# Kernel optimization log

Hardware: AMD Instinct MI355X
Metric: run time of the kernel (lower is better)

## Reference

```python
import jax, jax.numpy as jnp
import numpy as np

N_NODES = 50000
N_EDGES = 640000
N_REL = 8
D_IN = 128
D_HID = 128
D_OUT = 64


def setup_inputs() -> dict:
    key = jax.random.key(0)
    ks = jax.random.split(key, 10)
    x = jax.random.normal(ks[0], (N_NODES, D_IN), dtype=jnp.float32)
    edge_src = jax.random.randint(ks[1], (N_EDGES,), 0, N_NODES, dtype=jnp.int32)
    edge_dst = jax.random.randint(ks[2], (N_EDGES,), 0, N_NODES, dtype=jnp.int32)
    edge_type = jax.random.randint(ks[3], (N_EDGES,), 0, N_REL, dtype=jnp.int32)
    # Glorot-ish scaling for stability
    W1 = jax.random.normal(ks[4], (N_REL, D_IN, D_HID), dtype=jnp.float32) / np.sqrt(D_IN)
    root1 = jax.random.normal(ks[5], (D_IN, D_HID), dtype=jnp.float32) / np.sqrt(D_IN)
    b1 = jnp.zeros((D_HID,), dtype=jnp.float32)
    W2 = jax.random.normal(ks[6], (N_REL, D_HID, D_OUT), dtype=jnp.float32) / np.sqrt(D_HID)
    root2 = jax.random.normal(ks[7], (D_HID, D_OUT), dtype=jnp.float32) / np.sqrt(D_HID)
    b2 = jnp.zeros((D_OUT,), dtype=jnp.float32)
    return {"x": x, "edge_src": edge_src, "edge_dst": edge_dst, "edge_type": edge_type,
            "W1": W1, "root1": root1, "b1": b1, "W2": W2, "root2": root2, "b2": b2}


def rgcn_conv(x, edge_src, edge_dst, edge_type, W, W_root, b):
    """RGCNConv with default per-relation mean aggregation + root weight + bias."""
    N = x.shape[0]
    R, _, O = W.shape
    # Transform all nodes under all relation weights once: [N, R, O]
    xW = jnp.einsum('nd,rdo->nro', x, W)
    # Gather per-edge relation-specific messages: [E, O]
    msg = xW[edge_src, edge_type]
    # Segment per (dst, relation) for mean aggregation
    seg = edge_dst.astype(jnp.int32) * R + edge_type.astype(jnp.int32)
    cnt = jax.ops.segment_sum(jnp.ones_like(edge_type, dtype=x.dtype), seg, num_segments=N * R)
    agg = jax.ops.segment_sum(msg, seg, num_segments=N * R)  # [N*R, O]
    agg = agg / jnp.maximum(cnt, 1.0)[:, None]
    rel_sum = agg.reshape(N, R, O).sum(axis=1)  # [N, O]
    return rel_sum + x @ W_root + b


def reference(x, edge_src, edge_dst, edge_type, W1, root1, b1, W2, root2, b2):
    h = rgcn_conv(x, edge_src, edge_dst, edge_type, W1, root1, b1)
    h = rgcn_conv(h, edge_src, edge_dst, edge_type, W2, root2, b2)
    return jax.nn.sigmoid(h)
```

## Files before the change

### kernel.cpp

```cpp
#include <hip/hip_runtime.h>
#include <math.h>

#define NN 50000
#define NE 640000
#define NR 8
#define SCAN_N (NN * NR)
#define SCAN_CH 2048
#define SCAN_NB ((SCAN_N + SCAN_CH - 1) / SCAN_CH)

typedef __attribute__((ext_vector_type(8))) _Float16 half8;
typedef __attribute__((ext_vector_type(8))) short short8;
typedef __attribute__((ext_vector_type(4))) float f32x4;
typedef const void __attribute__((address_space(1))) gvoid_t;
typedef void __attribute__((address_space(3))) svoid_t;

__device__ __forceinline__ unsigned short f2h(float f) {
    _Float16 h = (_Float16)f;
    return __builtin_bit_cast(unsigned short, h);
}
__device__ __forceinline__ float h2f(unsigned short u) {
    return (float)__builtin_bit_cast(_Float16, u);
}

__global__ __launch_bounds__(256) void count_kernel(const int* __restrict__ dst,
                                                    const int* __restrict__ typ,
                                                    int* __restrict__ cnt, int E) {
    int e = blockIdx.x * 256 + threadIdx.x;
    if (e < E) atomicAdd(&cnt[dst[e] * NR + typ[e]], 1);
}

__global__ __launch_bounds__(256) void inv_kernel(const int* __restrict__ cnt,
                                                  float* __restrict__ inv, int n) {
    int i = blockIdx.x * 256 + threadIdx.x;
    if (i < n) {
        int c = cnt[i];
        inv[i] = 1.0f / (float)(c > 1 ? c : 1);
    }
}

__global__ __launch_bounds__(256) void scan1_kernel(const int* __restrict__ cnt,
                                                    int* __restrict__ loc,
                                                    int* __restrict__ bsum) {
    __shared__ int s[256];
    const int t = threadIdx.x;
    const int base = blockIdx.x * SCAN_CH + t * 8;
    int v[8];
    int sum = 0;
#pragma unroll
    for (int j = 0; j < 8; ++j) {
        int idx = base + j;
        v[j] = (idx < SCAN_N) ? cnt[idx] : 0;
        sum += v[j];
    }
    s[t] = sum;
    __syncthreads();
    for (int off = 1; off < 256; off <<= 1) {
        int u = (t >= off) ? s[t - off] : 0;
        __syncthreads();
        s[t] += u;
        __syncthreads();
    }
    int run = (t == 0) ? 0 : s[t - 1];
#pragma unroll
    for (int j = 0; j < 8; ++j) {
        int idx = base + j;
        if (idx < SCAN_N) loc[idx] = run;
        run += v[j];
    }
    if (t == 255) bsum[blockIdx.x] = s[255];
}

__global__ __launch_bounds__(256) void scan2_kernel(const int* __restrict__ bsum,
                                                    int* __restrict__ boff, int nb) {
    __shared__ int s[256];
    const int t = threadIdx.x;
    s[t] = (t < nb) ? bsum[t] : 0;
    __syncthreads();
    for (int off = 1; off < 256; off <<= 1) {
        int u = (t >= off) ? s[t - off] : 0;
        __syncthreads();
        s[t] += u;
        __syncthreads();
    }
    if (t < nb) boff[t] = (t == 0) ? 0 : s[t - 1];
    if (t == nb - 1) boff[nb] = s[t];
}

__global__ __launch_bounds__(256) void scan3_kernel(int* __restrict__ rowptr,
                                                    int* __restrict__ start,
                                                    const int* __restrict__ boff, int nb) {
    const int b = blockIdx.x, t = threadIdx.x;
    const int add = boff[b];
#pragma unroll
    for (int j = 0; j < 8; ++j) {
        int idx = b * SCAN_CH + t * 8 + j;
        if (idx < SCAN_N) {
            int v = rowptr[idx] + add;
            rowptr[idx] = v;
            start[idx] = v;
        }
    }
    if (b == 0 && t == 0) rowptr[SCAN_N] = boff[nb];
}

__global__ __launch_bounds__(256) void fill_kernel(const int* __restrict__ src,
                                                   const int* __restrict__ dst,
                                                   const int* __restrict__ typ,
                                                   int* __restrict__ start,
                                                   int* __restrict__ srcrel, int E) {
    int e = blockIdx.x * 256 + threadIdx.x;
    if (e >= E) return;
    int r = typ[e];
    int pos = atomicAdd(&start[dst[e] * NR + r], 1);
    srcrel[pos] = src[e] | (r << 20);
}

__global__ __launch_bounds__(256) void cvt_kernel(const float* __restrict__ x,
                                                  unsigned short* __restrict__ xh, int n4) {
    int i = blockIdx.x * 256 + threadIdx.x;
    if (i >= n4) return;
    float4 v = ((const float4*)x)[i];
    uint2 u;
    u.x = (unsigned)f2h(v.x) | ((unsigned)f2h(v.y) << 16);
    u.y = (unsigned)f2h(v.z) | ((unsigned)f2h(v.w) << 16);
    ((uint2*)xh)[i] = u;
}

__global__ __launch_bounds__(256) void pack_b_kernel(const float* __restrict__ W,
                                                     const float* __restrict__ root,
                                                     unsigned short* __restrict__ Bt, int O) {
    int i = blockIdx.x * 256 + threadIdx.x;
    int NTOT = 9 * O;
    if (i >= NTOT * 128) return;
    int k = i & 127, n = i >> 7;
    float v = (n < 8 * O) ? W[(size_t)(n / O) * 128 * O + (size_t)k * O + (n % O)]
                          : root[(size_t)k * O + (n - 8 * O)];
    Bt[(size_t)n * 128 + k] = f2h(v);
}

template <int LDC>
__global__ __launch_bounds__(256) void gemm_xw(const unsigned short* __restrict__ A,
                                               const unsigned short* __restrict__ Bt,
                                               unsigned short* __restrict__ C) {
    __shared__ __align__(16) unsigned short As[64 * 64];
    __shared__ __align__(16) unsigned short Bs[64 * 64];
    const int t = threadIdx.x;
    const int w = t >> 6, lane = t & 63;
    const int q = lane >> 4, m = lane & 15;
    const int wr = w >> 1, wc = w & 1;
    const int bm = blockIdx.y * 64;
    const int bn = blockIdx.x * 64;

    f32x4 acc[2][2];
#pragma unroll
    for (int mb = 0; mb < 2; ++mb)
#pragma unroll
        for (int nb = 0; nb < 2; ++nb) acc[mb][nb] = (f32x4)0.f;

    const int srow = lane >> 3, schk = lane & 7;

#pragma unroll
    for (int kc = 0; kc < 2; ++kc) {
        const int k0 = kc * 64;
#pragma unroll
        for (int ii = 0; ii < 2; ++ii) {
            int i = w * 2 + ii;
            int grow = bm + i * 8 + srow;
            if (grow >= NN) grow = NN - 1;
            const unsigned short* g = A + (size_t)grow * 128 + k0 + schk * 8;
            __builtin_amdgcn_global_load_lds((gvoid_t*)g, (svoid_t*)(As + i * 512), 16, 0, 0);
        }
#pragma unroll
        for (int ii = 0; ii < 2; ++ii) {
            int i = w * 2 + ii;
            const unsigned short* g = Bt + (size_t)(bn + i * 8 + srow) * 128 + k0 + schk * 8;
            __builtin_amdgcn_global_load_lds((gvoid_t*)g, (svoid_t*)(Bs + i * 512), 16, 0, 0);
        }
        __syncthreads();
#pragma unroll
        for (int s = 0; s < 2; ++s) {
            half8 af[2], bf[2];
#pragma unroll
            for (int mb = 0; mb < 2; ++mb)
                af[mb] = __builtin_bit_cast(half8,
                    *(const short8*)(As + (wr * 32 + mb * 16 + m) * 64 + s * 32 + q * 8));
#pragma unroll
            for (int nb = 0; nb < 2; ++nb)
                bf[nb] = __builtin_bit_cast(half8,
                    *(const short8*)(Bs + (wc * 32 + nb * 16 + m) * 64 + s * 32 + q * 8));
#pragma unroll
            for (int mb = 0; mb < 2; ++mb)
#pragma unroll
                for (int nb = 0; nb < 2; ++nb)
                    acc[mb][nb] = __builtin_amdgcn_mfma_f32_16x16x32_f16(af[mb], bf[nb],
                                                                         acc[mb][nb], 0, 0, 0);
        }
        __syncthreads();
    }

#pragma unroll
    for (int mb = 0; mb < 2; ++mb)
#pragma unroll
        for (int nb = 0; nb < 2; ++nb) {
            int col = bn + wc * 32 + nb * 16 + m;
#pragma unroll
            for (int j = 0; j < 4; ++j) {
                int grow = bm + wr * 32 + mb * 16 + q * 4 + j;
                if (grow < NN)
                    C[(size_t)grow * LDC + col] = f2h(acc[mb][nb][j]);
            }
        }
}

template <int O, bool FINAL>
__global__ __launch_bounds__(256) void agg_kernel(const int* __restrict__ rp,
                                                  const int* __restrict__ srcrel,
                                                  const float* __restrict__ inv,
                                                  const unsigned short* __restrict__ XW,
                                                  const float* __restrict__ bias,
                                                  void* __restrict__ Hout) {
    __shared__ float sinv[4][8];
    const int slot = threadIdx.x >> 6, lane = threadIdx.x & 63;
    const int w = blockIdx.x * 4 + slot;
    if (w >= NN) return;
    if (lane < 8) sinv[slot][lane] = inv[w * NR + lane];

    const int beg = rp[w * NR], end = rp[w * NR + NR];
    constexpr int LDC2 = 9 * O / 2;

    if (O == 128) {
        const unsigned int* X2 = (const unsigned int*)XW;
        float2 acc = make_float2(0.f, 0.f);
        int i = beg;
        for (; i + 3 < end; i += 4) {
            int p0 = srcrel[i], p1 = srcrel[i + 1], p2 = srcrel[i + 2], p3 = srcrel[i + 3];
            unsigned g0 = X2[(size_t)(p0 & 0xFFFFF) * LDC2 + (((unsigned)p0) >> 20) * 64 + lane];
            unsigned g1 = X2[(size_t)(p1 & 0xFFFFF) * LDC2 + (((unsigned)p1) >> 20) * 64 + lane];
            unsigned g2 = X2[(size_t)(p2 & 0xFFFFF) * LDC2 + (((unsigned)p2) >> 20) * 64 + lane];
            unsigned g3 = X2[(size_t)(p3 & 0xFFFFF) * LDC2 + (((unsigned)p3) >> 20) * 64 + lane];
            float s0 = sinv[slot][((unsigned)p0) >> 20];
            float s1 = sinv[slot][((unsigned)p1) >> 20];
            float s2 = sinv[slot][((unsigned)p2) >> 20];
            float s3 = sinv[slot][((unsigned)p3) >> 20];
            acc.x += h2f((unsigned short)(g0 & 0xFFFFu)) * s0;
            acc.y += h2f((unsigned short)(g0 >> 16)) * s0;
            acc.x += h2f((unsigned short)(g1 & 0xFFFFu)) * s1;
            acc.y += h2f((unsigned short)(g1 >> 16)) * s1;
            acc.x += h2f((unsigned short)(g2 & 0xFFFFu)) * s2;
            acc.y += h2f((unsigned short)(g2 >> 16)) * s2;
            acc.x += h2f((unsigned short)(g3 & 0xFFFFu)) * s3;
            acc.y += h2f((unsigned short)(g3 >> 16)) * s3;
        }
        for (; i < end; ++i) {
            int p0 = srcrel[i];
            unsigned g0 = X2[(size_t)(p0 & 0xFFFFF) * LDC2 + (((unsigned)p0) >> 20) * 64 + lane];
            float s0 = sinv[slot][((unsigned)p0) >> 20];
            acc.x += h2f((unsigned short)(g0 & 0xFFFFu)) * s0;
            acc.y += h2f((unsigned short)(g0 >> 16)) * s0;
        }
        unsigned rt = X2[(size_t)w * LDC2 + 512 + lane];
        float2 bv = ((const float2*)bias)[lane];
        float vx = acc.x + h2f((unsigned short)(rt & 0xFFFFu)) + bv.x;
        float vy = acc.y + h2f((unsigned short)(rt >> 16)) + bv.y;
        ((unsigned int*)Hout)[(size_t)w * 64 + lane] =
            (unsigned)f2h(vx) | ((unsigned)f2h(vy) << 16);
    } else {
        constexpr int LDC = 9 * O;
        float acc = 0.f;
        int i = beg;
        for (; i + 3 < end; i += 4) {
            int p0 = srcrel[i], p1 = srcrel[i + 1], p2 = srcrel[i + 2], p3 = srcrel[i + 3];
            unsigned short g0 = XW[(size_t)(p0 & 0xFFFFF) * LDC + (((unsigned)p0) >> 20) * 64 + lane];
            unsigned short g1 = XW[(size_t)(p1 & 0xFFFFF) * LDC + (((unsigned)p1) >> 20) * 64 + lane];
            unsigned short g2 = XW[(size_t)(p2 & 0xFFFFF) * LDC + (((unsigned)p2) >> 20) * 64 + lane];
            unsigned short g3 = XW[(size_t)(p3 & 0xFFFFF) * LDC + (((unsigned)p3) >> 20) * 64 + lane];
            acc += h2f(g0) * sinv[slot][((unsigned)p0) >> 20];
            acc += h2f(g1) * sinv[slot][((unsigned)p1) >> 20];
            acc += h2f(g2) * sinv[slot][((unsigned)p2) >> 20];
            acc += h2f(g3) * sinv[slot][((unsigned)p3) >> 20];
        }
        for (; i < end; ++i) {
            int p0 = srcrel[i];
            unsigned short g0 = XW[(size_t)(p0 & 0xFFFFF) * LDC + (((unsigned)p0) >> 20) * 64 + lane];
            acc += h2f(g0) * sinv[slot][((unsigned)p0) >> 20];
        }
        float v = acc + h2f(XW[(size_t)w * LDC + 512 + lane]) + bias[lane];
        ((float*)Hout)[(size_t)w * 64 + lane] = 1.f / (1.f + __expf(-v));
    }
}

extern "C" void kernel_launch(void* const* d_in, const int* in_sizes, int n_in,
                              void* d_out, int out_size, void* d_ws, size_t ws_size,
                              hipStream_t stream) {
    const float* x     = (const float*)d_in[0];
    const int*   esrc  = (const int*)d_in[1];
    const int*   edst  = (const int*)d_in[2];
    const int*   etyp  = (const int*)d_in[3];
    const float* W1    = (const float*)d_in[4];
    const float* root1 = (const float*)d_in[5];
    const float* b1    = (const float*)d_in[6];
    const float* W2    = (const float*)d_in[7];
    const float* root2 = (const float*)d_in[8];
    const float* b2    = (const float*)d_in[9];
    float* out = (float*)d_out;

    char* ws = (char*)d_ws;
    unsigned short* Bt1    = (unsigned short*)ws; ws += (size_t)1152 * 128 * 2;
    unsigned short* Bt2    = (unsigned short*)ws; ws += (size_t)576 * 128 * 2;
    int*            cnt    = (int*)ws;            ws += (size_t)SCAN_N * 4;
    float*          inv    = (float*)ws;          ws += (size_t)SCAN_N * 4;
    int*            rp     = (int*)ws;            ws += (size_t)(SCAN_N + 64) * 4;
    int*            start  = (int*)ws;            ws += (size_t)SCAN_N * 4;
    int*            bsum   = (int*)ws;            ws += (size_t)256 * 4;
    int*            boff   = (int*)ws;            ws += (size_t)257 * 4;
    int*            srcrel = (int*)ws;            ws += (size_t)NE * 4;
    unsigned short* xh     = (unsigned short*)ws; ws += (size_t)NN * 128 * 2;
    unsigned short* h1b    = (unsigned short*)ws; ws += (size_t)NN * 128 * 2;
    unsigned short* xW     = (unsigned short*)ws;
    unsigned short* xW2    = xW;

    hipMemsetAsync(cnt, 0, (size_t)SCAN_N * 4, stream);
    count_kernel<<<(NE + 255) / 256, 256, 0, stream>>>(edst, etyp, cnt, NE);
    inv_kernel<<<(SCAN_N + 255) / 256, 256, 0, stream>>>(cnt, inv, SCAN_N);
    scan1_kernel<<<SCAN_NB, 256, 0, stream>>>(cnt, rp, bsum);
    scan2_kernel<<<1, 256, 0, stream>>>(bsum, boff, SCAN_NB);
    scan3_kernel<<<SCAN_NB, 256, 0, stream>>>(rp, start, boff, SCAN_NB);
    fill_kernel<<<(NE + 255) / 256, 256, 0, stream>>>(esrc, edst, etyp, start, srcrel, NE);

    cvt_kernel<<<(NN * 32 + 255) / 256, 256, 0, stream>>>(x, xh, NN * 32);
    pack_b_kernel<<<(1152 * 128 + 255) / 256, 256, 0, stream>>>(W1, root1, Bt1, 128);
    pack_b_kernel<<<(576 * 128 + 255) / 256, 256, 0, stream>>>(W2, root2, Bt2, 64);

    const int agrid = (NN + 3) / 4;
    const int gy = (NN + 63) / 64;

    gemm_xw<1152><<<dim3(1152 / 64, gy), 256, 0, stream>>>(xh, Bt1, xW);
    agg_kernel<128, false><<<agrid, 256, 0, stream>>>(rp, srcrel, inv, xW, b1, h1b);

    gemm_xw<576><<<dim3(576 / 64, gy), 256, 0, stream>>>(h1b, Bt2, xW2);
    agg_kernel<64, true><<<agrid, 256, 0, stream>>>(rp, srcrel, inv, xW2, b2, out);
}
```

Measured before the change: 329.3 us.

## Fuse aggregation and transform: aggregate raw features per relation, then GEMM

```diff
diff --git a/kernel.cpp b/kernel.cpp
--- a/kernel.cpp
+++ b/kernel.cpp
@@ -11,8 +11,6 @@
 typedef __attribute__((ext_vector_type(8))) _Float16 half8;
 typedef __attribute__((ext_vector_type(8))) short short8;
 typedef __attribute__((ext_vector_type(4))) float f32x4;
-typedef const void __attribute__((address_space(1))) gvoid_t;
-typedef void __attribute__((address_space(3))) svoid_t;
 
 __device__ __forceinline__ unsigned short f2h(float f) {
     _Float16 h = (_Float16)f;
@@ -138,154 +136,136 @@
     Bt[(size_t)n * 128 + k] = f2h(v);
 }
 
-template <int LDC>
-__global__ __launch_bounds__(256) void gemm_xw(const unsigned short* __restrict__ A,
-                                               const unsigned short* __restrict__ Bt,
-                                               unsigned short* __restrict__ C) {
-    __shared__ __align__(16) unsigned short As[64 * 64];
-    __shared__ __align__(16) unsigned short Bs[64 * 64];
+#define ACC_EDGE(P, G)                                                        \
+    do {                                                                      \
+        unsigned r_ = ((unsigned)(P)) >> 20;                                  \
+        float vx_ = h2f((unsigned short)((G) & 0xFFFFu));                     \
+        float vy_ = h2f((unsigned short)((G) >> 16));                         \
+        switch (r_) {                                                         \
+            case 0: acc[0].x += vx_; acc[0].y += vy_; break;                  \
+            case 1: acc[1].x += vx_; acc[1].y += vy_; break;                  \
+            case 2: acc[2].x += vx_; acc[2].y += vy_; break;                  \
+            case 3: acc[3].x += vx_; acc[3].y += vy_; break;                  \
+            case 4: acc[4].x += vx_; acc[4].y += vy_; break;                  \
+            case 5: acc[5].x += vx_; acc[5].y += vy_; break;                  \
+            case 6: acc[6].x += vx_; acc[6].y += vy_; break;                  \
+            default: acc[7].x += vx_; acc[7].y += vy_; break;                 \
+        }                                                                     \
+    } while (0)
+
+template <int O, bool FINAL>
+__global__ __launch_bounds__(256, 2) void fused_layer(
+    const int* __restrict__ rp, const int* __restrict__ srcrel,
+    const float* __restrict__ inv, const unsigned short* __restrict__ X,
+    const unsigned short* __restrict__ Bt, const float* __restrict__ bias,
+    void* __restrict__ Hout) {
+    __shared__ __align__(16) unsigned short As[32 * 1024];
     const int t = threadIdx.x;
     const int w = t >> 6, lane = t & 63;
-    const int q = lane >> 4, m = lane & 15;
+    const int bm = blockIdx.x * 32;
+    const unsigned* X2 = (const unsigned*)X;
+
+    for (int i = 0; i < 8; ++i) {
+        const int m = w * 8 + i;
+        int d = bm + m;
+        if (d >= NN) d = NN - 1;
+        float2 acc[8];
+#pragma unroll
+        for (int r = 0; r < 8; ++r) acc[r] = make_float2(0.f, 0.f);
+
+        const int beg = rp[d * 8], end = rp[d * 8 + 8];
+        for (int base = beg; base < end; base += 64) {
+            int nv = end - base;
+            nv = nv > 64 ? 64 : nv;
+            int idx = base + (lane < nv ? lane : nv - 1);
+            int pv = srcrel[idx];
+            int j = 0;
+            for (; j + 3 < nv; j += 4) {
+                int p0 = __builtin_amdgcn_readlane(pv, j);
+                int p1 = __builtin_amdgcn_readlane(pv, j + 1);
+                int p2 = __builtin_amdgcn_readlane(pv, j + 2);
+                int p3 = __builtin_amdgcn_readlane(pv, j + 3);
+                unsigned g0 = X2[(p0 & 0xFFFFF) * 64 + lane];
+                unsigned g1 = X2[(p1 & 0xFFFFF) * 64 + lane];
+                unsigned g2 = X2[(p2 & 0xFFFFF) * 64 + lane];
+                unsigned g3 = X2[(p3 & 0xFFFFF) * 64 + lane];
+                ACC_EDGE(p0, g0);
+                ACC_EDGE(p1, g1);
+                ACC_EDGE(p2, g2);
+                ACC_EDGE(p3, g3);
+            }
+            for (; j < nv; ++j) {
+                int p0 = __builtin_amdgcn_readlane(pv, j);
+                unsigned g0 = X2[(p0 & 0xFFFFF) * 64 + lane];
+                ACC_EDGE(p0, g0);
+            }
+        }
+        char* rowp = (char*)As + m * 2048;
+        const int swz = (m & 7) << 4;
+#pragma unroll
+        for (int r = 0; r < 8; ++r) {
+            float iv = inv[d * 8 + r];
+            unsigned u = (unsigned)f2h(acc[r].x * iv) |
+                         ((unsigned)f2h(acc[r].y * iv) << 16);
+            *(unsigned*)(rowp + ((r * 256 + lane * 4) ^ swz)) = u;
+        }
+    }
+    __syncthreads();
+
     const int wr = w >> 1, wc = w & 1;
-    const int bm = blockIdx.y * 64;
-    const int bn = blockIdx.x * 64;
-
-    f32x4 acc[2][2];
-#pragma unroll
-    for (int mb = 0; mb < 2; ++mb)
-#pragma unroll
-        for (int nb = 0; nb < 2; ++nb) acc[mb][nb] = (f32x4)0.f;
-
-    const int srow = lane >> 3, schk = lane & 7;
-
-#pragma unroll
-    for (int kc = 0; kc < 2; ++kc) {
-        const int k0 = kc * 64;
-#pragma unroll
-        for (int ii = 0; ii < 2; ++ii) {
-            int i = w * 2 + ii;
-            int grow = bm + i * 8 + srow;
-            if (grow >= NN) grow = NN - 1;
-            const unsigned short* g = A + (size_t)grow * 128 + k0 + schk * 8;
-            __builtin_amdgcn_global_load_lds((gvoid_t*)g, (svoid_t*)(As + i * 512), 16, 0, 0);
-        }
-#pragma unroll
-        for (int ii = 0; ii < 2; ++ii) {
-            int i = w * 2 + ii;
-            const unsigned short* g = Bt + (size_t)(bn + i * 8 + srow) * 128 + k0 + schk * 8;
-            __builtin_amdgcn_global_load_lds((gvoid_t*)g, (svoid_t*)(Bs + i * 512), 16, 0, 0);
-        }
-        __syncthreads();
-#pragma unroll
-        for (int s = 0; s < 2; ++s) {
-            half8 af[2], bf[2];
-#pragma unroll
-            for (int mb = 0; mb < 2; ++mb)
-                af[mb] = __builtin_bit_cast(half8,
-                    *(const short8*)(As + (wr * 32 + mb * 16 + m) * 64 + s * 32 + q * 8));
-#pragma unroll
-            for (int nb = 0; nb < 2; ++nb)
-                bf[nb] = __builtin_bit_cast(half8,
-                    *(const short8*)(Bs + (wc * 32 + nb * 16 + m) * 64 + s * 32 + q * 8));
-#pragma unroll
-            for (int mb = 0; mb < 2; ++mb)
-#pragma unroll
-                for (int nb = 0; nb < 2; ++nb)
-                    acc[mb][nb] = __builtin_amdgcn_mfma_f32_16x16x32_f16(af[mb], bf[nb],
-                                                                         acc[mb][nb], 0, 0, 0);
-        }
-        __syncthreads();
-    }
-
-#pragma unroll
-    for (int mb = 0; mb < 2; ++mb)
-#pragma unroll
-        for (int nb = 0; nb < 2; ++nb) {
-            int col = bn + wc * 32 + nb * 16 + m;
-#pragma unroll
-            for (int j = 0; j < 4; ++j) {
-                int grow = bm + wr * 32 + mb * 16 + q * 4 + j;
-                if (grow < NN)
-                    C[(size_t)grow * LDC + col] = f2h(acc[mb][nb][j]);
-            }
-        }
-}
-
-template <int O, bool FINAL>
-__global__ __launch_bounds__(256) void agg_kernel(const int* __restrict__ rp,
-                                                  const int* __restrict__ srcrel,
-                                                  const float* __restrict__ inv,
-                                                  const unsigned short* __restrict__ XW,
-                                                  const float* __restrict__ bias,
-                                                  void* __restrict__ Hout) {
-    __shared__ float sinv[4][8];
-    const int slot = threadIdx.x >> 6, lane = threadIdx.x & 63;
-    const int w = blockIdx.x * 4 + slot;
-    if (w >= NN) return;
-    if (lane < 8) sinv[slot][lane] = inv[w * NR + lane];
-
-    const int beg = rp[w * NR], end = rp[w * NR + NR];
-    constexpr int LDC2 = 9 * O / 2;
-
-    if (O == 128) {
-        const unsigned int* X2 = (const unsigned int*)XW;
-        float2 acc = make_float2(0.f, 0.f);
-        int i = beg;
-        for (; i + 3 < end; i += 4) {
-            int p0 = srcrel[i], p1 = srcrel[i + 1], p2 = srcrel[i + 2], p3 = srcrel[i + 3];
-            unsigned g0 = X2[(size_t)(p0 & 0xFFFFF) * LDC2 + (((unsigned)p0) >> 20) * 64 + lane];
-            unsigned g1 = X2[(size_t)(p1 & 0xFFFFF) * LDC2 + (((unsigned)p1) >> 20) * 64 + lane];
-            unsigned g2 = X2[(size_t)(p2 & 0xFFFFF) * LDC2 + (((unsigned)p2) >> 20) * 64 + lane];
-            unsigned g3 = X2[(size_t)(p3 & 0xFFFFF) * LDC2 + (((unsigned)p3) >> 20) * 64 + lane];
-            float s0 = sinv[slot][((unsigned)p0) >> 20];
-            float s1 = sinv[slot][((unsigned)p1) >> 20];
-            float s2 = sinv[slot][((unsigned)p2) >> 20];
-            float s3 = sinv[slot][((unsigned)p3) >> 20];
-            acc.x += h2f((unsigned short)(g0 & 0xFFFFu)) * s0;
-            acc.y += h2f((unsigned short)(g0 >> 16)) * s0;
-            acc.x += h2f((unsigned short)(g1 & 0xFFFFu)) * s1;
-            acc.y += h2f((unsigned short)(g1 >> 16)) * s1;
-            acc.x += h2f((unsigned short)(g2 & 0xFFFFu)) * s2;
-            acc.y += h2f((unsigned short)(g2 >> 16)) * s2;
-            acc.x += h2f((unsigned short)(g3 & 0xFFFFu)) * s3;
-            acc.y += h2f((unsigned short)(g3 >> 16)) * s3;
-        }
-        for (; i < end; ++i) {
-            int p0 = srcrel[i];
-            unsigned g0 = X2[(size_t)(p0 & 0xFFFFF) * LDC2 + (((unsigned)p0) >> 20) * 64 + lane];
-            float s0 = sinv[slot][((unsigned)p0) >> 20];
-            acc.x += h2f((unsigned short)(g0 & 0xFFFFu)) * s0;
-            acc.y += h2f((unsigned short)(g0 >> 16)) * s0;
-        }
-        unsigned rt = X2[(size_t)w * LDC2 + 512 + lane];
-        float2 bv = ((const float2*)bias)[lane];
-        float vx = acc.x + h2f((unsigned short)(rt & 0xFFFFu)) + bv.x;
-        float vy = acc.y + h2f((unsigned short)(rt >> 16)) + bv.y;
-        ((unsigned int*)Hout)[(size_t)w * 64 + lane] =
-            (unsigned)f2h(vx) | ((unsigned)f2h(vy) << 16);
-    } else {
-        constexpr int LDC = 9 * O;
-        float acc = 0.f;
-        int i = beg;
-        for (; i + 3 < end; i += 4) {
-            int p0 = srcrel[i], p1 = srcrel[i + 1], p2 = srcrel[i + 2], p3 = srcrel[i + 3];
-            unsigned short g0 = XW[(size_t)(p0 & 0xFFFFF) * LDC + (((unsigned)p0) >> 20) * 64 + lane];
-            unsigned short g1 = XW[(size_t)(p1 & 0xFFFFF) * LDC + (((unsigned)p1) >> 20) * 64 + lane];
-            unsigned short g2 = XW[(size_t)(p2 & 0xFFFFF) * LDC + (((unsigned)p2) >> 20) * 64 + lane];
-            unsigned short g3 = XW[(size_t)(p3 & 0xFFFFF) * LDC + (((unsigned)p3) >> 20) * 64 + lane];
-            acc += h2f(g0) * sinv[slot][((unsigned)p0) >> 20];
-            acc += h2f(g1) * sinv[slot][((unsigned)p1) >> 20];
-            acc += h2f(g2) * sinv[slot][((unsigned)p2) >> 20];
-            acc += h2f(g3) * sinv[slot][((unsigned)p3) >> 20];
-        }
-        for (; i < end; ++i) {
-            int p0 = srcrel[i];
-            unsigned short g0 = XW[(size_t)(p0 & 0xFFFFF) * LDC + (((unsigned)p0) >> 20) * 64 + lane];
-            acc += h2f(g0) * sinv[slot][((unsigned)p0) >> 20];
-        }
-        float v = acc + h2f(XW[(size_t)w * LDC + 512 + lane]) + bias[lane];
-        ((float*)Hout)[(size_t)w * 64 + lane] = 1.f / (1.f + __expf(-v));
+    const int q = lane >> 4, ml = lane & 15;
+    constexpr int NT = O / 32;
+    f32x4 accv[NT];
+#pragma unroll
+    for (int nt = 0; nt < NT; ++nt) accv[nt] = (f32x4)0.f;
+
+    const int arow = wr * 16 + ml;
+    int aglob = bm + arow;
+    if (aglob >= NN) aglob = NN - 1;
+    const unsigned short* Xroot = X + (size_t)aglob * 128;
+    const char* arowp = (const char*)As + arow * 2048;
+    const int aswz = (arow & 7) << 4;
+
+#pragma unroll
+    for (int r = 0; r < 9; ++r) {
+#pragma unroll
+        for (int kk = 0; kk < 4; ++kk) {
+            half8 af;
+            if (r < 8) {
+                af = __builtin_bit_cast(
+                    half8, *(const short8*)(arowp +
+                                            ((r * 256 + kk * 64 + q * 16) ^ aswz)));
+            } else {
+                af = __builtin_bit_cast(half8,
+                                        *(const short8*)(Xroot + kk * 32 + q * 8));
+            }
+#pragma unroll
+            for (int nt = 0; nt < NT; ++nt) {
+                const unsigned short* bp =
+                    Bt + (size_t)(r * O + wc * (O / 2) + nt * 16 + ml) * 128 +
+                    kk * 32 + q * 8;
+                half8 bf = __builtin_bit_cast(half8, *(const short8*)bp);
+                accv[nt] = __builtin_amdgcn_mfma_f32_16x16x32_f16(af, bf, accv[nt],
+                                                                  0, 0, 0);
+            }
+        }
+    }
+
+#pragma unroll
+    for (int nt = 0; nt < NT; ++nt) {
+        int col = wc * (O / 2) + nt * 16 + ml;
+        float bv = bias[col];
+#pragma unroll
+        for (int j = 0; j < 4; ++j) {
+            int grow = bm + wr * 16 + q * 4 + j;
+            if (grow < NN) {
+                float v = accv[nt][j] + bv;
+                if (FINAL)
+                    ((float*)Hout)[(size_t)grow * O + col] = 1.f / (1.f + __expf(-v));
+                else
+                    ((unsigned short*)Hout)[(size_t)grow * O + col] = f2h(v);
+            }
+        }
     }
 }
 
@@ -315,9 +295,7 @@
     int*            boff   = (int*)ws;            ws += (size_t)257 * 4;
     int*            srcrel = (int*)ws;            ws += (size_t)NE * 4;
     unsigned short* xh     = (unsigned short*)ws; ws += (size_t)NN * 128 * 2;
-    unsigned short* h1b    = (unsigned short*)ws; ws += (size_t)NN * 128 * 2;
-    unsigned short* xW     = (unsigned short*)ws;
-    unsigned short* xW2    = xW;
+    unsigned short* h1b    = (unsigned short*)ws;
 
     hipMemsetAsync(cnt, 0, (size_t)SCAN_N * 4, stream);
     count_kernel<<<(NE + 255) / 256, 256, 0, stream>>>(edst, etyp, cnt, NE);
@@ -331,12 +309,8 @@
     pack_b_kernel<<<(1152 * 128 + 255) / 256, 256, 0, stream>>>(W1, root1, Bt1, 128);
     pack_b_kernel<<<(576 * 128 + 255) / 256, 256, 0, stream>>>(W2, root2, Bt2, 64);
 
-    const int agrid = (NN + 3) / 4;
-    const int gy = (NN + 63) / 64;
-
-    gemm_xw<1152><<<dim3(1152 / 64, gy), 256, 0, stream>>>(xh, Bt1, xW);
-    agg_kernel<128, false><<<agrid, 256, 0, stream>>>(rp, srcrel, inv, xW, b1, h1b);
-
-    gemm_xw<576><<<dim3(576 / 64, gy), 256, 0, stream>>>(h1b, Bt2, xW2);
-    agg_kernel<64, true><<<agrid, 256, 0, stream>>>(rp, srcrel, inv, xW2, b2, out);
-}
+    const int fgrid = (NN + 31) / 32;
+
+    fused_layer<128, false><<<fgrid, 256, 0, stream>>>(rp, srcrel, inv, xh, Bt1, b1, h1b);
+    fused_layer<64, true><<<fgrid, 256, 0, stream>>>(rp, srcrel, inv, h1b, Bt2, b2, out);
+}
```

After: 603.6 us. +83.3%, slower.
